# Performance work log

Hardware: AMD Instinct MI355X
Metric: run time of the kernel (lower is better)

The kernel has to match this reference:

```python
import jax, jax.numpy as jnp
import numpy as np
from jax import lax


def conv2d(x, w, b):
    # NCHW valid conv, stride 1 (matches torch Conv2d defaults)
    y = lax.conv_general_dilated(x, w, (1, 1), 'VALID',
                                 dimension_numbers=('NCHW', 'OIHW', 'NCHW'))
    return y + b[None, :, None, None]


def maxpool2(x):
    return lax.reduce_window(x, -jnp.inf, lax.max, (1, 1, 2, 2), (1, 1, 2, 2), 'VALID')


def affine_grid(theta, H, W):
    # F.affine_grid(theta, size, align_corners=True): base coords linspace(-1,1)
    xs = jnp.linspace(-1.0, 1.0, W, dtype=theta.dtype)
    ys = jnp.linspace(-1.0, 1.0, H, dtype=theta.dtype)
    gy, gx = jnp.meshgrid(ys, xs, indexing='ij')
    base = jnp.stack([gx, gy, jnp.ones_like(gx)], axis=-1)  # [H,W,3]
    return jnp.einsum('bij,hwj->bhwi', theta, base)  # [B,H,W,2] (x,y)


def grid_sample_bilinear(x, grid):
    # F.grid_sample(x, grid, mode='bilinear', padding_mode='zeros', align_corners=True)
    B, C, H, W = x.shape
    ix = (grid[..., 0] + 1.0) * 0.5 * (W - 1)  # [B,H,W]
    iy = (grid[..., 1] + 1.0) * 0.5 * (H - 1)
    x0 = jnp.floor(ix); y0 = jnp.floor(iy)
    x1 = x0 + 1.0;      y1 = y0 + 1.0

    def gather(yc, xc):
        yi = jnp.clip(yc, 0, H - 1).astype(jnp.int32)
        xi = jnp.clip(xc, 0, W - 1).astype(jnp.int32)
        # per-batch advanced-index gather -> [B,C,Hg,Wg]
        return jax.vmap(lambda img, yy, xx: img[:, yy, xx])(x, yi, xi)

    def valid(yc, xc):
        return ((xc >= 0) & (xc <= W - 1) & (yc >= 0) & (yc <= H - 1)).astype(x.dtype)

    w00 = (x1 - ix) * (y1 - iy)
    w01 = (ix - x0) * (y1 - iy)
    w10 = (x1 - ix) * (iy - y0)
    w11 = (ix - x0) * (iy - y0)
    out = (gather(y0, x0) * (w00 * valid(y0, x0))[:, None]
           + gather(y0, x1) * (w01 * valid(y0, x1))[:, None]
           + gather(y1, x0) * (w10 * valid(y1, x0))[:, None]
           + gather(y1, x1) * (w11 * valid(y1, x1))[:, None])
    return out


def setup_inputs() -> dict:
    key = jax.random.key(0)
    ks = jax.random.split(key, 8)
    B, C, H, W = 128, 3, 224, 224
    LOC_SIZE = 10 * 52 * 52  # 27040, from conv/pool arithmetic on 224x224
    x = jax.random.normal(ks[0], (B, C, H, W), dtype=jnp.float32)
    conv1_w = jax.random.normal(ks[1], (8, C, 7, 7), dtype=jnp.float32) * (1.0 / np.sqrt(C * 49))
    conv1_b = jnp.zeros((8,), dtype=jnp.float32)
    conv2_w = jax.random.normal(ks[2], (10, 8, 5, 5), dtype=jnp.float32) * (1.0 / np.sqrt(8 * 25))
    conv2_b = jnp.zeros((10,), dtype=jnp.float32)
    fc1_w = jax.random.normal(ks[3], (32, LOC_SIZE), dtype=jnp.float32) * (1.0 / np.sqrt(LOC_SIZE))
    fc1_b = jnp.zeros((32,), dtype=jnp.float32)
    fc2_w = jax.random.normal(ks[4], (6, 32), dtype=jnp.float32) * 0.01
    fc2_b = jnp.array([1.0, 0.0, 0.0, 0.0, 1.0, 0.0], dtype=jnp.float32)
    return {"x": x, "conv1_w": conv1_w, "conv1_b": conv1_b,
            "conv2_w": conv2_w, "conv2_b": conv2_b,
            "fc1_w": fc1_w, "fc1_b": fc1_b, "fc2_w": fc2_w, "fc2_b": fc2_b}


def reference(x, conv1_w, conv1_b, conv2_w, conv2_b, fc1_w, fc1_b, fc2_w, fc2_b):
    B, C, H, W = x.shape
    # localization net
    xs = jax.nn.relu(maxpool2(conv2d(x, conv1_w, conv1_b)))
    xs = jax.nn.relu(maxpool2(conv2d(xs, conv2_w, conv2_b)))
    xs = xs.reshape(B, -1)  # [B, 27040]
    h = jax.nn.relu(xs @ fc1_w.T + fc1_b)
    theta = (h @ fc2_w.T + fc2_b).reshape(-1, 2, 3)
    grid = affine_grid(theta, H, W)
    return grid_sample_bilinear(x, grid)
```

## Files before the change

### kernel.cpp

```cpp
#include <hip/hip_runtime.h>
#include <hip/hip_bf16.h>
#include <stdint.h>

typedef __bf16 bf16x8 __attribute__((ext_vector_type(8)));
typedef float f32x4 __attribute__((ext_vector_type(4)));
typedef unsigned long long u64;

union BFrag { uint32_t u[4]; u64 q[2]; bf16x8 v; };
union R16 { uint4 v; u64 q[2]; };

__device__ __forceinline__ void split1(float f, uint32_t& hi, uint32_t& lo) {
  uint32_t b = __float_as_uint(f);
  hi = b >> 16;
  float fl = f - __uint_as_float(b & 0xFFFF0000u);
  lo = __float_as_uint(fl) >> 16;
}

__global__ __launch_bounds__(256) void k0_wprep(
    const float* __restrict__ w1, const float* __restrict__ w2,
    unsigned short* __restrict__ wpHi, unsigned short* __restrict__ wpLo,
    unsigned short* __restrict__ wp2Hi, unsigned short* __restrict__ wp2Lo) {
  int id = blockIdx.x * 256 + threadIdx.x;
  if (id < 4096) {
    int j = id & 7, n = (id >> 3) & 15, g = (id >> 7) & 3, jf = id >> 9;
    int o = n & 7, half = n >> 3;
    int ky = jf - half, c = j & 3, kx = 2 * g + (j >> 2);
    float f = 0.f;
    if (c < 3 && kx < 7 && ky >= 0 && ky < 7)
      f = w1[o * 147 + c * 49 + ky * 7 + kx];
    uint32_t h, l;
    split1(f, h, l);
    wpHi[id] = (unsigned short)h;
    wpLo[id] = (unsigned short)l;
  }
  if (id < 5120) {
    int j = id & 7, n = (id >> 3) & 15, g = (id >> 7) & 3;
    int hk = id >> 9;
    int h = hk & 1, ky = hk >> 1;
    int c = 4 * h + (j & 3), kx = 2 * g + (j >> 2);
    float f = 0.f;
    if (n < 10 && kx < 5)
      f = w2[n * 200 + c * 25 + ky * 5 + kx];
    uint32_t hh, ll;
    split1(f, hh, ll);
    wp2Hi[id] = (unsigned short)hh;
    wp2Lo[id] = (unsigned short)ll;
  }
}

__global__ __launch_bounds__(512) void k1_mfma(
    const float* __restrict__ x, const unsigned short* __restrict__ wpHi,
    const unsigned short* __restrict__ wpLo, const float* __restrict__ bias,
    float* __restrict__ out) {
  __shared__ unsigned short sI[70 * 40 * 8];
  const int b = blockIdx.z;
  const int x0 = blockIdx.x * 32;
  const int y0blk = blockIdx.y * 64;
  const int tid = threadIdx.x;
  const int lane = tid & 63, wid = tid >> 6;
  const int n = lane & 15, g = lane >> 4;
  const int xh = wid & 1, yq = wid >> 1;

  BFrag bhi[8], blo[8];
#pragma unroll
  for (int jf = 0; jf < 8; ++jf) {
    uint4 th = *(const uint4*)&wpHi[((jf * 4 + g) * 16 + n) * 8];
    uint4 tl = *(const uint4*)&wpLo[((jf * 4 + g) * 16 + n) * 8];
    bhi[jf].u[0] = th.x; bhi[jf].u[1] = th.y;
    bhi[jf].u[2] = th.z; bhi[jf].u[3] = th.w;
    blo[jf].u[0] = tl.x; blo[jf].u[1] = tl.y;
    blo[jf].u[2] = tl.z; blo[jf].u[3] = tl.w;
  }

  const float* xb = x + (size_t)b * 3 * 50176;
  float pv0[6], pv1[6], pv2[6];
#pragma unroll
  for (int u = 0; u < 6; ++u) {
    int pos = tid + u * 512;
    if (pos < 2800) {
      int row = pos / 40, col = pos % 40;
      int gy = y0blk + row; gy = gy < 223 ? gy : 223;
      int gx = x0 + col;    gx = gx < 223 ? gx : 223;
      const float* p = xb + (size_t)gy * 224 + gx;
      pv0[u] = p[0];
      pv1[u] = p[50176];
      pv2[u] = p[100352];
    }
  }
#pragma unroll
  for (int u = 0; u < 6; ++u) {
    int pos = tid + u * 512;
    if (pos < 2800) {
      uint32_t h0, l0, h1, l1, h2, l2;
      split1(pv0[u], h0, l0);
      split1(pv1[u], h1, l1);
      split1(pv2[u], h2, l2);
      uint4 q;
      q.x = h0 | (h1 << 16);
      q.y = h2;
      q.z = l0 | (l1 << 16);
      q.w = l2;
      *(uint4*)&sI[pos * 8] = q;
    }
  }
  __syncthreads();

  const int y0w = y0blk + yq * 16;
  if (y0w <= 217) {
    f32x4 acc[8];
#pragma unroll
    for (int i = 0; i < 8; ++i) acc[i] = (f32x4){0.f, 0.f, 0.f, 0.f};

    const int mg = xh * 16 + n + 2 * g;
    const int rbase = yq * 16;
#pragma unroll
    for (int t = 0; t < 22; ++t) {
      const int s0 = ((rbase + t) * 40 + mg) * 8;
      R16 r0, r1;
      r0.v = *(const uint4*)&sI[s0];
      r1.v = *(const uint4*)&sI[s0 + 8];
      BFrag ah, al;
      ah.q[0] = r0.q[0]; al.q[0] = r0.q[1];
      ah.q[1] = r1.q[0]; al.q[1] = r1.q[1];
#pragma unroll
      for (int i = 0; i < 8; ++i) {
        const int jf = t - 2 * i;
        if (jf >= 0 && jf < 8)
          acc[i] = __builtin_amdgcn_mfma_f32_16x16x32_bf16(ah.v, bhi[jf].v, acc[i], 0, 0, 0);
      }
#pragma unroll
      for (int i = 0; i < 8; ++i) {
        const int jf = t - 2 * i;
        if (jf >= 0 && jf < 8)
          acc[i] = __builtin_amdgcn_mfma_f32_16x16x32_bf16(ah.v, blo[jf].v, acc[i], 0, 0, 0);
      }
#pragma unroll
      for (int i = 0; i < 8; ++i) {
        const int jf = t - 2 * i;
        if (jf >= 0 && jf < 8)
          acc[i] = __builtin_amdgcn_mfma_f32_16x16x32_bf16(al.v, bhi[jf].v, acc[i], 0, 0, 0);
      }
    }

    const int o = n & 7;
    const float bs = bias[o];
    const int px0 = x0 / 2 + xh * 8 + 2 * g;
    const int py0 = y0w / 2;
#pragma unroll
    for (int i = 0; i < 8; ++i) {
      float v0 = fmaxf(acc[i][0], acc[i][1]);
      float v1 = fmaxf(acc[i][2], acc[i][3]);
      float p0 = __shfl_xor(v0, 8, 64);
      float p1 = __shfl_xor(v1, 8, 64);
      const int py = py0 + i;
      if (n < 8 && py < 109) {
        float m0 = fmaxf(v0, p0) + bs;
        float m1 = fmaxf(v1, p1) + bs;
        float* op = out + (((size_t)(b * 109 + py)) * 109 + px0) * 8 + o;
        if (px0 < 109)     op[0] = fmaxf(m0, 0.f);
        if (px0 + 1 < 109) op[8] = fmaxf(m1, 0.f);
      }
    }
  }
}

__global__ __launch_bounds__(128) void k2_mfma(
    const float* __restrict__ in, const unsigned short* __restrict__ wpHi,
    const unsigned short* __restrict__ wpLo, const float* __restrict__ bias,
    float* __restrict__ out) {
  __shared__ unsigned short sI[20 * 24 * 16];
  const int b = blockIdx.z;
  const int px0 = (blockIdx.x < 6) ? blockIdx.x * 8 : 44;
  const int py0 = (blockIdx.y < 6) ? blockIdx.y * 8 : 44;
  const int x0c = px0 * 2, y0c = py0 * 2;
  const int tid = threadIdx.x;
  const int lane = tid & 63, wid = tid >> 6;
  const int n = lane & 15, g = lane >> 4;

  const float* ib = in + (size_t)b * 109 * 109 * 8;
  float v[4][8];
#pragma unroll
  for (int u = 0; u < 4; ++u) {
    int pos = tid + u * 128;
    if (pos < 480) {
      int row = pos / 24, col = pos % 24;
      int gy = y0c + row;
      int gx = x0c + col; gx = gx < 108 ? gx : 108;
      const float* p = ib + ((size_t)gy * 109 + gx) * 8;
      float4 q0 = *(const float4*)p;
      float4 q1 = *(const float4*)(p + 4);
      v[u][0] = q0.x; v[u][1] = q0.y; v[u][2] = q0.z; v[u][3] = q0.w;
      v[u][4] = q1.x; v[u][5] = q1.y; v[u][6] = q1.z; v[u][7] = q1.w;
    }
  }
#pragma unroll
  for (int u = 0; u < 4; ++u) {
    int pos = tid + u * 128;
    if (pos < 480) {
      uint32_t hh[8], ll[8];
#pragma unroll
      for (int c = 0; c < 8; ++c) split1(v[u][c], hh[c], ll[c]);
      uint4 q0, q1;
      q0.x = hh[0] | (hh[1] << 16); q0.y = hh[2] | (hh[3] << 16);
      q0.z = ll[0] | (ll[1] << 16); q0.w = ll[2] | (ll[3] << 16);
      q1.x = hh[4] | (hh[5] << 16); q1.y = hh[6] | (hh[7] << 16);
      q1.z = ll[4] | (ll[5] << 16); q1.w = ll[6] | (ll[7] << 16);
      *(uint4*)&sI[pos * 16] = q0;
      *(uint4*)&sI[pos * 16 + 8] = q1;
    }
  }
  __syncthreads();

  f32x4 acc[8];
#pragma unroll
  for (int i = 0; i < 8; ++i) acc[i] = (f32x4){0.f, 0.f, 0.f, 0.f};

  const int mg = n + 2 * g;
  const int rbase = wid * 8;
#pragma unroll
  for (int h = 0; h < 2; ++h) {
    BFrag bh[5], bl[5];
#pragma unroll
    for (int ky = 0; ky < 5; ++ky) {
      int idx = (((ky * 2 + h) * 4 + g) * 16 + n) * 8;
      uint4 th = *(const uint4*)&wpHi[idx];
      uint4 tl = *(const uint4*)&wpLo[idx];
      bh[ky].u[0] = th.x; bh[ky].u[1] = th.y;
      bh[ky].u[2] = th.z; bh[ky].u[3] = th.w;
      bl[ky].u[0] = tl.x; bl[ky].u[1] = tl.y;
      bl[ky].u[2] = tl.z; bl[ky].u[3] = tl.w;
    }
#pragma unroll
    for (int t = 0; t < 12; ++t) {
      const int s0 = ((rbase + t) * 24 + mg) * 16 + h * 8;
      R16 r0, r1;
      r0.v = *(const uint4*)&sI[s0];
      r1.v = *(const uint4*)&sI[s0 + 16];
      BFrag ah, al;
      ah.q[0] = r0.q[0]; al.q[0] = r0.q[1];
      ah.q[1] = r1.q[0]; al.q[1] = r1.q[1];
#pragma unroll
      for (int ky = 0; ky < 5; ++ky) {
        const int i = t - ky;
        if (i >= 0 && i < 8)
          acc[i] = __builtin_amdgcn_mfma_f32_16x16x32_bf16(ah.v, bh[ky].v, acc[i], 0, 0, 0);
      }
#pragma unroll
      for (int ky = 0; ky < 5; ++ky) {
        const int i = t - ky;
        if (i >= 0 && i < 8)
          acc[i] = __builtin_amdgcn_mfma_f32_16x16x32_bf16(ah.v, bl[ky].v, acc[i], 0, 0, 0);
      }
#pragma unroll
      for (int ky = 0; ky < 5; ++ky) {
        const int i = t - ky;
        if (i >= 0 && i < 8)
          acc[i] = __builtin_amdgcn_mfma_f32_16x16x32_bf16(al.v, bh[ky].v, acc[i], 0, 0, 0);
      }
    }
  }

  if (n < 10) {
    const float bs = bias[n];
    const int pxb = px0 + 2 * g;
    const int pyb = py0 + wid * 4;
#pragma unroll
    for (int u = 0; u < 4; ++u) {
      f32x4 A0 = acc[2 * u], A1 = acc[2 * u + 1];
      float m0 = fmaxf(fmaxf(A0[0], A0[1]), fmaxf(A1[0], A1[1])) + bs;
      float m1 = fmaxf(fmaxf(A0[2], A0[3]), fmaxf(A1[2], A1[3])) + bs;
      float* op = out + ((size_t)(b * 10 + n) * 52 + pyb + u) * 52 + pxb;
      op[0] = fmaxf(m0, 0.f);
      op[1] = fmaxf(m1, 0.f);
    }
  }
}

__global__ __launch_bounds__(256) void k3_fc1_partial(
    const float* __restrict__ xs, const float* __restrict__ w,
    float* __restrict__ part) {
  __shared__ float sA[128 * 64];
  __shared__ float sW[64 * 33];
  const int p = blockIdx.x;
  const int tid = threadIdx.x;
  const int n = tid & 31, bg = tid >> 5;
  float acc[16];
#pragma unroll
  for (int i = 0; i < 16; ++i) acc[i] = 0.f;

  for (int ch = 0; ch < 2; ++ch) {
    const int k0 = p * 128 + ch * 64;
    __syncthreads();
#pragma unroll
    for (int bb = 0; bb < 4; ++bb) {
      float v[8];
#pragma unroll
      for (int u = 0; u < 8; ++u) {
        int idx = bb * 2048 + u * 256 + tid;
        int bbv = idx >> 6, k = idx & 63;
        int gk = k0 + k;
        v[u] = (gk < 27040) ? xs[bbv * 27040 + gk] : 0.f;
      }
#pragma unroll
      for (int u = 0; u < 8; ++u) {
        int idx = bb * 2048 + u * 256 + tid;
        sA[idx] = v[u];
      }
    }
    {
      float v[8];
#pragma unroll
      for (int u = 0; u < 8; ++u) {
        int idx = u * 256 + tid;
        int nn = idx >> 6, k = idx & 63;
        int gk = k0 + k;
        v[u] = (gk < 27040) ? w[nn * 27040 + gk] : 0.f;
      }
#pragma unroll
      for (int u = 0; u < 8; ++u) {
        int idx = u * 256 + tid;
        int nn = idx >> 6, k = idx & 63;
        sW[k * 33 + nn] = v[u];
      }
    }
    __syncthreads();
    for (int k = 0; k < 64; k += 4) {
      float w0 = sW[(k + 0) * 33 + n];
      float w1 = sW[(k + 1) * 33 + n];
      float w2 = sW[(k + 2) * 33 + n];
      float w3 = sW[(k + 3) * 33 + n];
#pragma unroll
      for (int i = 0; i < 16; ++i) {
        float4 a = *(const float4*)&sA[(bg * 16 + i) * 64 + k];
        acc[i] = fmaf(a.x, w0, acc[i]);
        acc[i] = fmaf(a.y, w1, acc[i]);
        acc[i] = fmaf(a.z, w2, acc[i]);
        acc[i] = fmaf(a.w, w3, acc[i]);
      }
    }
  }
#pragma unroll
  for (int i = 0; i < 16; ++i)
    part[p * 4096 + (bg * 16 + i) * 32 + n] = acc[i];
}

__global__ __launch_bounds__(256) void k4_reduce(
    const float* __restrict__ part, const float* __restrict__ b1,
    float* __restrict__ h) {
  const int lane = threadIdx.x & 31;
  const int eloc = threadIdx.x >> 5;
  const int e = blockIdx.x * 8 + eloc;
  float s = 0.f;
#pragma unroll
  for (int pc = 0; pc < 8; ++pc) s += part[(pc * 32 + lane) * 4096 + e];
#pragma unroll
  for (int off = 16; off > 0; off >>= 1) s += __shfl_down(s, off, 32);
  if (lane == 0) h[e] = fmaxf(s + b1[e & 31], 0.f);
}

__global__ __launch_bounds__(256) void k5_sample(
    const float* __restrict__ x, const float* __restrict__ h,
    const float* __restrict__ w2, const float* __restrict__ b2,
    float* __restrict__ out) {
  __shared__ float th[6];
  const int b = blockIdx.z;
  if (threadIdx.x < 6) {
    int j = threadIdx.x;
    float s = b2[j];
    for (int m = 0; m < 32; ++m) s = fmaf(h[b * 32 + m], w2[j * 32 + m], s);
    th[j] = s;
  }
  __syncthreads();

  const int pix = blockIdx.x * 256 + threadIdx.x;
  const int hh = pix / 224, ww = pix % 224;
  const float step = 2.0f / 223.0f;
  float gx = ww * step - 1.0f, gy = hh * step - 1.0f;
  float tx = th[0] * gx + th[1] * gy + th[2];
  float ty = th[3] * gx + th[4] * gy + th[5];
  float ix = (tx + 1.0f) * 0.5f * 223.0f;
  float iy = (ty + 1.0f) * 0.5f * 223.0f;
  float x0 = floorf(ix), y0 = floorf(iy);
  float x1 = x0 + 1.f, y1 = y0 + 1.f;
  float wx1 = ix - x0, wx0 = x1 - ix;
  float wy1 = iy - y0, wy0 = y1 - iy;
  float w00 = wx0 * wy0, w01 = wx1 * wy0, w10 = wx0 * wy1, w11 = wx1 * wy1;
  bool vx0 = (x0 >= 0.f) && (x0 <= 223.f);
  bool vx1 = (x1 >= 0.f) && (x1 <= 223.f);
  bool vy0 = (y0 >= 0.f) && (y0 <= 223.f);
  bool vy1 = (y1 >= 0.f) && (y1 <= 223.f);
  w00 = (vx0 && vy0) ? w00 : 0.f;
  w01 = (vx1 && vy0) ? w01 : 0.f;
  w10 = (vx0 && vy1) ? w10 : 0.f;
  w11 = (vx1 && vy1) ? w11 : 0.f;
  int xi0 = (int)fminf(fmaxf(x0, 0.f), 223.f);
  int xi1 = (int)fminf(fmaxf(x1, 0.f), 223.f);
  int yi0 = (int)fminf(fmaxf(y0, 0.f), 223.f);
  int yi1 = (int)fminf(fmaxf(y1, 0.f), 223.f);
#pragma unroll
  for (int c = 0; c < 3; ++c) {
    const float* img = x + (size_t)((b * 3 + c) * 224) * 224;
    float v = img[yi0 * 224 + xi0] * w00 + img[yi0 * 224 + xi1] * w01 +
              img[yi1 * 224 + xi0] * w10 + img[yi1 * 224 + xi1] * w11;
    out[((b * 3 + c) * 224 + hh) * 224 + ww] = v;
  }
}

extern "C" void kernel_launch(void* const* d_in, const int* in_sizes, int n_in,
                              void* d_out, int out_size, void* d_ws,
                              size_t ws_size, hipStream_t stream) {
  const float* x   = (const float*)d_in[0];
  const float* w1  = (const float*)d_in[1];
  const float* b1  = (const float*)d_in[2];
  const float* w2  = (const float*)d_in[3];
  const float* b2  = (const float*)d_in[4];
  const float* fw1 = (const float*)d_in[5];
  const float* fb1 = (const float*)d_in[6];
  const float* fw2 = (const float*)d_in[7];
  const float* fb2 = (const float*)d_in[8];
  float* out = (float*)d_out;

  float* ws   = (float*)d_ws;
  float* out1 = ws;
  float* xs   = out1 + 12166144;
  float* part = xs + 3461120;
  float* hbuf = part + 1048576;
  unsigned short* wpHi  = (unsigned short*)(hbuf + 4096);
  unsigned short* wpLo  = wpHi + 4096;
  unsigned short* wp2Hi = wpLo + 4096;
  unsigned short* wp2Lo = wp2Hi + 5120;

  k0_wprep<<<20, 256, 0, stream>>>(w1, w2, wpHi, wpLo, wp2Hi, wp2Lo);
  k1_mfma<<<dim3(7, 4, 128), 512, 0, stream>>>(x, wpHi, wpLo, b1, out1);
  k2_mfma<<<dim3(7, 7, 128), 128, 0, stream>>>(out1, wp2Hi, wp2Lo, b2, xs);
  k3_fc1_partial<<<256, 256, 0, stream>>>(xs, fw1, part);
  k4_reduce<<<512, 256, 0, stream>>>(part, fb1, hbuf);
  k5_sample<<<dim3(196, 1, 128), 256, 0, stream>>>(x, hbuf, fw2, fb2, out);
}
```

Baseline: 186.2 us.

## Retile conv2 kernel into wide 16x4 pooled tiles with four waves

Reshapes the conv2 MFMA kernel's output tile from 8x8 pooled pixels with 2 waves to 16 wide by 4 tall pooled pixels with 4 waves, each wave covering an 8x2 sub-tile. The grid becomes 4x13 blocks per image with no overlapping edge tiles in y. Weight fragments are now loaded in two groups of kernel rows to reduce register pressure. The halo overhead per block grows (12 input rows for 4 output rows), so shared-memory fill work per output rises in exchange for more parallelism and fewer accumulators per wave.

```diff
diff --git a/kernel.cpp b/kernel.cpp
--- a/kernel.cpp
+++ b/kernel.cpp
@@ -164,26 +164,28 @@
   }
 }
 
-__global__ __launch_bounds__(128) void k2_mfma(
+__global__ __launch_bounds__(256) void k2_mfma(
     const float* __restrict__ in, const unsigned short* __restrict__ wpHi,
     const unsigned short* __restrict__ wpLo, const float* __restrict__ bias,
     float* __restrict__ out) {
-  __shared__ unsigned short sI[20 * 24 * 16];
+  __shared__ unsigned short sI[12 * 40 * 16];
   const int b = blockIdx.z;
-  const int px0 = (blockIdx.x < 6) ? blockIdx.x * 8 : 44;
-  const int py0 = (blockIdx.y < 6) ? blockIdx.y * 8 : 44;
+  const int bx = blockIdx.x;
+  const int px0 = (bx < 3) ? bx * 16 : 36;
+  const int py0 = blockIdx.y * 4;
   const int x0c = px0 * 2, y0c = py0 * 2;
   const int tid = threadIdx.x;
   const int lane = tid & 63, wid = tid >> 6;
   const int n = lane & 15, g = lane >> 4;
+  const int xh = wid & 1, yw = wid >> 1;
 
   const float* ib = in + (size_t)b * 109 * 109 * 8;
-  float v[4][8];
-#pragma unroll
-  for (int u = 0; u < 4; ++u) {
-    int pos = tid + u * 128;
+  float v[2][8];
+#pragma unroll
+  for (int u = 0; u < 2; ++u) {
+    int pos = tid + u * 256;
     if (pos < 480) {
-      int row = pos / 24, col = pos % 24;
+      int row = pos / 40, col = pos % 40;
       int gy = y0c + row;
       int gx = x0c + col; gx = gx < 108 ? gx : 108;
       const float* p = ib + ((size_t)gy * 109 + gx) * 8;
@@ -194,8 +196,8 @@
     }
   }
 #pragma unroll
-  for (int u = 0; u < 4; ++u) {
-    int pos = tid + u * 128;
+  for (int u = 0; u < 2; ++u) {
+    int pos = tid + u * 256;
     if (pos < 480) {
       uint32_t hh[8], ll[8];
 #pragma unroll
@@ -211,61 +213,77 @@
   }
   __syncthreads();
 
-  f32x4 acc[8];
-#pragma unroll
-  for (int i = 0; i < 8; ++i) acc[i] = (f32x4){0.f, 0.f, 0.f, 0.f};
-
-  const int mg = n + 2 * g;
-  const int rbase = wid * 8;
+  f32x4 acc[4];
+#pragma unroll
+  for (int i = 0; i < 4; ++i) acc[i] = (f32x4){0.f, 0.f, 0.f, 0.f};
+
+  const int mg = xh * 16 + n + 2 * g;
+  const int rbase = yw * 4;
 #pragma unroll
   for (int h = 0; h < 2; ++h) {
-    BFrag bh[5], bl[5];
-#pragma unroll
-    for (int ky = 0; ky < 5; ++ky) {
-      int idx = (((ky * 2 + h) * 4 + g) * 16 + n) * 8;
-      uint4 th = *(const uint4*)&wpHi[idx];
-      uint4 tl = *(const uint4*)&wpLo[idx];
-      bh[ky].u[0] = th.x; bh[ky].u[1] = th.y;
-      bh[ky].u[2] = th.z; bh[ky].u[3] = th.w;
-      bl[ky].u[0] = tl.x; bl[ky].u[1] = tl.y;
-      bl[ky].u[2] = tl.z; bl[ky].u[3] = tl.w;
-    }
-#pragma unroll
-    for (int t = 0; t < 12; ++t) {
-      const int s0 = ((rbase + t) * 24 + mg) * 16 + h * 8;
-      R16 r0, r1;
-      r0.v = *(const uint4*)&sI[s0];
-      r1.v = *(const uint4*)&sI[s0 + 16];
-      BFrag ah, al;
-      ah.q[0] = r0.q[0]; al.q[0] = r0.q[1];
-      ah.q[1] = r1.q[0]; al.q[1] = r1.q[1];
-#pragma unroll
-      for (int ky = 0; ky < 5; ++ky) {
-        const int i = t - ky;
-        if (i >= 0 && i < 8)
-          acc[i] = __builtin_amdgcn_mfma_f32_16x16x32_bf16(ah.v, bh[ky].v, acc[i], 0, 0, 0);
-      }
-#pragma unroll
-      for (int ky = 0; ky < 5; ++ky) {
-        const int i = t - ky;
-        if (i >= 0 && i < 8)
-          acc[i] = __builtin_amdgcn_mfma_f32_16x16x32_bf16(ah.v, bl[ky].v, acc[i], 0, 0, 0);
-      }
-#pragma unroll
-      for (int ky = 0; ky < 5; ++ky) {
-        const int i = t - ky;
-        if (i >= 0 && i < 8)
-          acc[i] = __builtin_amdgcn_mfma_f32_16x16x32_bf16(al.v, bh[ky].v, acc[i], 0, 0, 0);
+#pragma unroll
+    for (int kyg = 0; kyg < 2; ++kyg) {
+      const int ky0 = kyg ? 3 : 0;
+      const int nky = kyg ? 2 : 3;
+      BFrag bh[3], bl[3];
+#pragma unroll
+      for (int k = 0; k < 3; ++k) {
+        if (k < nky) {
+          int idx = ((((ky0 + k) * 2 + h) * 4 + g) * 16 + n) * 8;
+          uint4 th = *(const uint4*)&wpHi[idx];
+          uint4 tl = *(const uint4*)&wpLo[idx];
+          bh[k].u[0] = th.x; bh[k].u[1] = th.y;
+          bh[k].u[2] = th.z; bh[k].u[3] = th.w;
+          bl[k].u[0] = tl.x; bl[k].u[1] = tl.y;
+          bl[k].u[2] = tl.z; bl[k].u[3] = tl.w;
+        }
+      }
+#pragma unroll
+      for (int t = 0; t < 8; ++t) {
+        const bool anyUse = kyg ? (t >= 3) : (t <= 5);
+        if (anyUse) {
+          const int s0 = ((rbase + t) * 40 + mg) * 16 + h * 8;
+          R16 r0, r1;
+          r0.v = *(const uint4*)&sI[s0];
+          r1.v = *(const uint4*)&sI[s0 + 16];
+          BFrag ah, al;
+          ah.q[0] = r0.q[0]; al.q[0] = r0.q[1];
+          ah.q[1] = r1.q[0]; al.q[1] = r1.q[1];
+#pragma unroll
+          for (int k = 0; k < 3; ++k) {
+            if (k < nky) {
+              const int i = t - (ky0 + k);
+              if (i >= 0 && i < 4)
+                acc[i] = __builtin_amdgcn_mfma_f32_16x16x32_bf16(ah.v, bh[k].v, acc[i], 0, 0, 0);
+            }
+          }
+#pragma unroll
+          for (int k = 0; k < 3; ++k) {
+            if (k < nky) {
+              const int i = t - (ky0 + k);
+              if (i >= 0 && i < 4)
+                acc[i] = __builtin_amdgcn_mfma_f32_16x16x32_bf16(ah.v, bl[k].v, acc[i], 0, 0, 0);
+            }
+          }
+#pragma unroll
+          for (int k = 0; k < 3; ++k) {
+            if (k < nky) {
+              const int i = t - (ky0 + k);
+              if (i >= 0 && i < 4)
+                acc[i] = __builtin_amdgcn_mfma_f32_16x16x32_bf16(al.v, bh[k].v, acc[i], 0, 0, 0);
+            }
+          }
+        }
       }
     }
   }
 
   if (n < 10) {
     const float bs = bias[n];
-    const int pxb = px0 + 2 * g;
-    const int pyb = py0 + wid * 4;
-#pragma unroll
-    for (int u = 0; u < 4; ++u) {
+    const int pxb = px0 + xh * 8 + 2 * g;
+    const int pyb = py0 + yw * 2;
+#pragma unroll
+    for (int u = 0; u < 2; ++u) {
       f32x4 A0 = acc[2 * u], A1 = acc[2 * u + 1];
       float m0 = fmaxf(fmaxf(A0[0], A0[1]), fmaxf(A1[0], A1[1])) + bs;
       float m1 = fmaxf(fmaxf(A0[2], A0[3]), fmaxf(A1[2], A1[3])) + bs;
@@ -432,7 +450,7 @@
 
   k0_wprep<<<20, 256, 0, stream>>>(w1, w2, wpHi, wpLo, wp2Hi, wp2Lo);
   k1_mfma<<<dim3(7, 4, 128), 512, 0, stream>>>(x, wpHi, wpLo, b1, out1);
-  k2_mfma<<<dim3(7, 7, 128), 128, 0, stream>>>(out1, wp2Hi, wp2Lo, b2, xs);
+  k2_mfma<<<dim3(4, 13, 128), 256, 0, stream>>>(out1, wp2Hi, wp2Lo, b2, xs);
   k3_fc1_partial<<<256, 256, 0, stream>>>(xs, fw1, part);
   k4_reduce<<<512, 256, 0, stream>>>(part, fb1, hbuf);
   k5_sample<<<dim3(196, 1, 128), 256, 0, stream>>>(x, hbuf, fw2, fb2, out);
```

After: 187.7 us. Within noise of the previous version (+0.8%).
